# Optimization experiments

Hardware: AMD Instinct MI355X
Metric: run time of the kernel (lower is better)

The kernel has to match this reference:

```python
import jax, jax.numpy as jnp
import numpy as np
from jax import lax

T, IN, H, OUT = 8192, 1, 1024, 1


def setup_inputs() -> dict:
    key = jax.random.key(0)
    ks = jax.random.split(key, 7)
    s = 1.0 / np.sqrt(H)
    return {
        "x": jax.random.normal(ks[0], (T, IN), dtype=jnp.float32),
        "W_ih": jax.random.uniform(ks[1], (4 * H, IN), jnp.float32, -s, s),
        "W_hh": jax.random.uniform(ks[2], (4 * H, H), jnp.float32, -s, s),
        "b_ih": jax.random.uniform(ks[3], (4 * H,), jnp.float32, -s, s),
        "b_hh": jax.random.uniform(ks[4], (4 * H,), jnp.float32, -s, s),
        "W_fc": jax.random.uniform(ks[5], (OUT, H), jnp.float32, -s, s),
        "b_fc": jax.random.uniform(ks[6], (OUT,), jnp.float32, -s, s),
    }


def reference(x, W_ih, W_hh, b_ih, b_hh, W_fc, b_fc):
    # x: (T, input_size); batch dim of 1 is squeezed out.
    H_ = W_hh.shape[1]
    # Precompute input contribution to all gates for every timestep: (T, 4H)
    xg = x @ W_ih.T + (b_ih + b_hh)

    def step(carry, gx):
        h, c = carry
        g = gx + h @ W_hh.T  # (4H,) -- PyTorch gate order i, f, g, o
        i, f, gg, o = jnp.split(g, 4)
        c = jax.nn.sigmoid(f) * c + jax.nn.sigmoid(i) * jnp.tanh(gg)
        h = jax.nn.sigmoid(o) * jnp.tanh(c)
        return (h, c), h

    h0 = jnp.zeros((H_,), dtype=x.dtype)
    c0 = jnp.zeros((H_,), dtype=x.dtype)
    _, hs = lax.scan(step, (h0, c0), xg)  # hs: (T, H)
    return hs @ W_fc.T + b_fc  # (T, output_size)
```

## Files before the change

kernel.cpp:

```cpp
#include <hip/hip_runtime.h>

#define TT    8192
#define HD    1024
#define NBLK  256
#define NTHR  256
#define NBUF  4
#define NREP  8

typedef int i32x4 __attribute__((ext_vector_type(4)));
typedef int i32x2 __attribute__((ext_vector_type(2)));

__device__ __forceinline__ void llc_load_pair(const unsigned* p, i32x4& a, i32x4& b) {
  asm volatile("global_load_dwordx4 %0, %2, off sc0 sc1\n\t"
               "global_load_dwordx4 %1, %3, off sc0 sc1\n\t"
               "s_waitcnt vmcnt(0)"
               : "=&v"(a), "=&v"(b)
               : "v"(p), "v"(p + 4)
               : "memory");
}
__device__ __forceinline__ unsigned llc_load1(const unsigned* p) {
  unsigned r;
  asm volatile("global_load_dword %0, %1, off sc0 sc1\n\ts_waitcnt vmcnt(0)"
               : "=v"(r) : "v"(p) : "memory");
  return r;
}
__device__ __forceinline__ void llc_store2(unsigned* p, unsigned lo, unsigned hi) {
  i32x2 v; v.x = (int)lo; v.y = (int)hi;
  asm volatile("global_store_dwordx2 %0, %1, off sc0 sc1"
               :: "v"(p), "v"(v) : "memory");
}
__device__ __forceinline__ void llc_store1(unsigned* p, unsigned v) {
  asm volatile("global_store_dword %0, %1, off sc0 sc1"
               :: "v"(p), "v"(v) : "memory");
}

__device__ __forceinline__ float sigf(float z) {
  return 1.0f / (1.0f + __expf(-z));
}
__device__ __forceinline__ float tanh_fast(float z) {
  float az = fabsf(z);
  float e  = __expf(2.0f * az);
  float t  = 1.0f - 2.0f / (e + 1.0f);
  return z < 0.0f ? -t : t;
}

#define FMA4(acc, hvv, wvv)                                      \
  acc = fmaf((hvv).x, (wvv).x, acc);                             \
  acc = fmaf((hvv).y, (wvv).y, acc);                             \
  acc = fmaf((hvv).z, (wvv).z, acc);                             \
  acc = fmaf((hvv).w, (wvv).w, acc);

extern "C" __global__ __launch_bounds__(NTHR, 1)
void lstm_persistent(const float* __restrict__ x,
                     const float* __restrict__ W_ih,
                     const float* __restrict__ W_hh,
                     const float* __restrict__ b_ih,
                     const float* __restrict__ b_hh,
                     const float* __restrict__ W_fc,
                     const float* __restrict__ b_fc,
                     float* __restrict__ out,
                     unsigned* __restrict__ flag,
                     unsigned* __restrict__ hbuf)
{
  const int tid = threadIdx.x;
  const int blk = blockIdx.x;

  if (blk == NBLK) {
    for (int t = 0; t < TT; ++t) {
      const unsigned* src = hbuf + (((t & (NBUF - 1)) * HD + tid * 4) * 2);
      i32x4 A, B;
      const int want = t + 1;
      do {
        llc_load_pair(src, A, B);
      } while (!(A.y == want && A.w == want && B.y == want && B.w == want));
      __syncthreads();
      if (tid < NREP)
        llc_store1(flag + (tid << 4), (unsigned)want);
    }
    return;
  }

  __shared__ float x_lds[TT];
  __shared__ float h_lds[HD];

  const int wave = tid >> 6;
  const int lane = tid & 63;
  const int g    = lane >> 4;
  const int kc   = lane & 15;
  const int unit = blk * 4 + wave;

  for (int i = tid; i < TT / 4; i += NTHR)
    ((float4*)x_lds)[i] = ((const float4*)x)[i];

  float4 w4[16];
  {
    const float* wr = W_hh + (size_t)(g * HD + unit) * HD + kc * 4;
#pragma unroll
    for (int m = 0; m < 16; ++m)
      w4[m] = *((const float4*)(wr + m * 64));
  }
  float4 wfc4[4];
#pragma unroll
  for (int m = 0; m < 4; ++m)
    wfc4[m] = *((const float4*)(W_fc + m * 256 + lane * 4));
  const float bfc_val = b_fc[0];

  float wih_g[4], bs_g[4];
#pragma unroll
  for (int q = 0; q < 4; ++q) {
    int r = q * HD + unit;
    wih_g[q] = W_ih[r];
    bs_g[q]  = b_ih[r] + b_hh[r];
  }
  float c_state = 0.0f;
  __syncthreads();

  const unsigned* flag_mine = flag + ((blk & (NREP - 1)) << 4);

  for (int t = 0; t < TT; ++t) {
    const bool doproj = (t > 0) && (wave == 1) && (blk == (t & 255));
    float accs = 0.0f;
    float4 hp4[4];

    if (t > 0) {
      while (llc_load1(flag_mine) < (unsigned)t) { }
      const unsigned* src = hbuf + (((t - 1) & (NBUF - 1)) * HD + tid * 4) * 2;
      i32x4 A, B;
      llc_load_pair(src, A, B);
      float4 hv;
      hv.x = __int_as_float(A.x); hv.y = __int_as_float(A.z);
      hv.z = __int_as_float(B.x); hv.w = __int_as_float(B.z);
      ((float4*)h_lds)[tid] = hv;
      __syncthreads();

      const float* hp = h_lds + kc * 4;
      float s0 = 0.f, s1 = 0.f, s2 = 0.f, s3 = 0.f;
#pragma unroll
      for (int mb = 0; mb < 4; ++mb) {
        float4 ha = *((const float4*)(hp + (mb * 4 + 0) * 64));
        float4 hb = *((const float4*)(hp + (mb * 4 + 1) * 64));
        float4 hc = *((const float4*)(hp + (mb * 4 + 2) * 64));
        float4 hd = *((const float4*)(hp + (mb * 4 + 3) * 64));
        FMA4(s0, ha, w4[mb * 4 + 0]);
        FMA4(s1, hb, w4[mb * 4 + 1]);
        FMA4(s2, hc, w4[mb * 4 + 2]);
        FMA4(s3, hd, w4[mb * 4 + 3]);
      }
      accs = (s0 + s1) + (s2 + s3);

      if (doproj) {
#pragma unroll
        for (int m = 0; m < 4; ++m)
          hp4[m] = *((const float4*)(h_lds + m * 256 + lane * 4));
      }
    }

#pragma unroll
    for (int s = 1; s < 16; s <<= 1)
      accs += __shfl_xor(accs, s);

    float xt = x_lds[t];
    float a  = accs + fmaf(xt, wih_g[g], bs_g[g]);
    float act = (g == 2) ? tanh_fast(a) : sigf(a);

    float si = __shfl(act, 0);
    float sf = __shfl(act, 16);
    float sg = __shfl(act, 32);
    float so = __shfl(act, 48);

    if (lane == 0) {
      c_state  = sf * c_state + si * sg;
      float hn = so * tanh_fast(c_state);
      llc_store2(hbuf + (((t & (NBUF - 1)) * HD + unit) * 2),
                 __float_as_uint(hn), (unsigned)(t + 1));
    }

    if (doproj) {
      float p = 0.f;
#pragma unroll
      for (int m = 0; m < 4; ++m) { FMA4(p, hp4[m], wfc4[m]); }
#pragma unroll
      for (int s = 1; s < 64; s <<= 1) p += __shfl_xor(p, s);
      if (lane == 0) out[t - 1] = p + bfc_val;
    }
  }

  if (blk == 0) {
    const unsigned* src = hbuf + (((TT - 1) & (NBUF - 1)) * HD + tid * 4) * 2;
    i32x4 A, B;
    do {
      llc_load_pair(src, A, B);
    } while (!(A.y == TT && A.w == TT && B.y == TT && B.w == TT));
    float4 hv;
    hv.x = __int_as_float(A.x); hv.y = __int_as_float(A.z);
    hv.z = __int_as_float(B.x); hv.w = __int_as_float(B.z);
    ((float4*)h_lds)[tid] = hv;
    __syncthreads();
    if (wave == 1) {
      float p = 0.f;
#pragma unroll
      for (int m = 0; m < 4; ++m) {
        float4 hm = *((const float4*)(h_lds + m * 256 + lane * 4));
        FMA4(p, hm, wfc4[m]);
      }
#pragma unroll
      for (int s = 1; s < 64; s <<= 1) p += __shfl_xor(p, s);
      if (lane == 0) out[TT - 1] = p + bfc_val;
    }
  }
}

extern "C" void kernel_launch(void* const* d_in, const int* in_sizes, int n_in,
                              void* d_out, int out_size, void* d_ws, size_t ws_size,
                              hipStream_t stream) {
  const float* x   = (const float*)d_in[0];
  const float* Wih = (const float*)d_in[1];
  const float* Whh = (const float*)d_in[2];
  const float* bih = (const float*)d_in[3];
  const float* bhh = (const float*)d_in[4];
  const float* Wfc = (const float*)d_in[5];
  const float* bfc = (const float*)d_in[6];
  float* out = (float*)d_out;

  unsigned* flag = (unsigned*)d_ws;
  unsigned* hbuf = flag + NREP * 16;
  size_t init_bytes = (NREP * 16 + NBUF * HD * 2) * sizeof(unsigned);

  hipMemsetAsync(d_ws, 0, init_bytes, stream);
  hipLaunchKernelGGL(lstm_persistent, dim3(NBLK + 1), dim3(NTHR), 0, stream,
                     x, Wih, Whh, bih, bhh, Wfc, bfc, out, flag, hbuf);
}
```

Before: 23.23 ms.

## Speculatively poll tagged h buffer and distribute output projection via atomics

Each block first polls the tagged hidden-state entries directly, up to KSPEC attempts, and falls back to the aggregator flag only if that fails. This aims to remove the extra hop through the aggregator block from the per-step critical path. Each block's own h values are taken from LDS instead of global memory. The serial output projection, previously done by one rotating block, becomes per-block partial dot products accumulated with atomicAdd into a zeroed output. The cost is an extra __syncthreads per step, 256 atomics per timestep on the same address, and heavier polling traffic on the LLC.

```diff
diff --git a/kernel.cpp b/kernel.cpp
--- a/kernel.cpp
+++ b/kernel.cpp
@@ -6,6 +6,7 @@
 #define NTHR  256
 #define NBUF  4
 #define NREP  8
+#define KSPEC 4
 
 typedef int i32x4 __attribute__((ext_vector_type(4)));
 typedef int i32x2 __attribute__((ext_vector_type(2)));
@@ -69,19 +70,21 @@
     for (int t = 0; t < TT; ++t) {
       const unsigned* src = hbuf + (((t & (NBUF - 1)) * HD + tid * 4) * 2);
       i32x4 A, B;
-      const int want = t + 1;
+      const unsigned want = (unsigned)(t + 1);
       do {
         llc_load_pair(src, A, B);
-      } while (!(A.y == want && A.w == want && B.y == want && B.w == want));
+      } while (!((unsigned)A.y >= want && (unsigned)A.w >= want &&
+                 (unsigned)B.y >= want && (unsigned)B.w >= want));
       __syncthreads();
       if (tid < NREP)
-        llc_store1(flag + (tid << 4), (unsigned)want);
+        llc_store1(flag + (tid << 4), want);
     }
     return;
   }
 
   __shared__ float x_lds[TT];
   __shared__ float h_lds[HD];
+  __shared__ float own_h[4];
 
   const int wave = tid >> 6;
   const int lane = tid & 63;
@@ -99,12 +102,6 @@
     for (int m = 0; m < 16; ++m)
       w4[m] = *((const float4*)(wr + m * 64));
   }
-  float4 wfc4[4];
-#pragma unroll
-  for (int m = 0; m < 4; ++m)
-    wfc4[m] = *((const float4*)(W_fc + m * 256 + lane * 4));
-  const float bfc_val = b_fc[0];
-
   float wih_g[4], bs_g[4];
 #pragma unroll
   for (int q = 0; q < 4; ++q) {
@@ -112,24 +109,42 @@
     wih_g[q] = W_ih[r];
     bs_g[q]  = b_ih[r] + b_hh[r];
   }
+  float wfco[4];
+#pragma unroll
+  for (int q = 0; q < 4; ++q) wfco[q] = W_fc[blk * 4 + q];
+  const float bfc_add = (blk == 0) ? b_fc[0] : 0.0f;
+
   float c_state = 0.0f;
   __syncthreads();
 
   const unsigned* flag_mine = flag + ((blk & (NREP - 1)) << 4);
 
   for (int t = 0; t < TT; ++t) {
-    const bool doproj = (t > 0) && (wave == 1) && (blk == (t & 255));
     float accs = 0.0f;
-    float4 hp4[4];
 
     if (t > 0) {
-      while (llc_load1(flag_mine) < (unsigned)t) { }
-      const unsigned* src = hbuf + (((t - 1) & (NBUF - 1)) * HD + tid * 4) * 2;
-      i32x4 A, B;
-      llc_load_pair(src, A, B);
+      const unsigned want = (unsigned)t;
       float4 hv;
-      hv.x = __int_as_float(A.x); hv.y = __int_as_float(A.z);
-      hv.z = __int_as_float(B.x); hv.w = __int_as_float(B.z);
+      if (tid == blk) {
+        hv.x = own_h[0]; hv.y = own_h[1]; hv.z = own_h[2]; hv.w = own_h[3];
+      } else {
+        const unsigned* src =
+            hbuf + (((t - 1) & (NBUF - 1)) * HD + tid * 4) * 2;
+        i32x4 A, B;
+        bool ok;
+        int att = 0;
+        do {
+          llc_load_pair(src, A, B);
+          ok = ((unsigned)A.y == want && (unsigned)A.w == want &&
+                (unsigned)B.y == want && (unsigned)B.w == want);
+        } while (!ok && ++att < KSPEC);
+        if (!ok) {
+          while (llc_load1(flag_mine) < want) { }
+          llc_load_pair(src, A, B);
+        }
+        hv.x = __int_as_float(A.x); hv.y = __int_as_float(A.z);
+        hv.z = __int_as_float(B.x); hv.w = __int_as_float(B.z);
+      }
       ((float4*)h_lds)[tid] = hv;
       __syncthreads();
 
@@ -147,12 +162,6 @@
         FMA4(s3, hd, w4[mb * 4 + 3]);
       }
       accs = (s0 + s1) + (s2 + s3);
-
-      if (doproj) {
-#pragma unroll
-        for (int m = 0; m < 4; ++m)
-          hp4[m] = *((const float4*)(h_lds + m * 256 + lane * 4));
-      }
     }
 
 #pragma unroll
@@ -173,39 +182,15 @@
       float hn = so * tanh_fast(c_state);
       llc_store2(hbuf + (((t & (NBUF - 1)) * HD + unit) * 2),
                  __float_as_uint(hn), (unsigned)(t + 1));
-    }
-
-    if (doproj) {
-      float p = 0.f;
-#pragma unroll
-      for (int m = 0; m < 4; ++m) { FMA4(p, hp4[m], wfc4[m]); }
-#pragma unroll
-      for (int s = 1; s < 64; s <<= 1) p += __shfl_xor(p, s);
-      if (lane == 0) out[t - 1] = p + bfc_val;
-    }
-  }
-
-  if (blk == 0) {
-    const unsigned* src = hbuf + (((TT - 1) & (NBUF - 1)) * HD + tid * 4) * 2;
-    i32x4 A, B;
-    do {
-      llc_load_pair(src, A, B);
-    } while (!(A.y == TT && A.w == TT && B.y == TT && B.w == TT));
-    float4 hv;
-    hv.x = __int_as_float(A.x); hv.y = __int_as_float(A.z);
-    hv.z = __int_as_float(B.x); hv.w = __int_as_float(B.z);
-    ((float4*)h_lds)[tid] = hv;
+      own_h[wave] = hn;
+    }
+
     __syncthreads();
-    if (wave == 1) {
-      float p = 0.f;
-#pragma unroll
-      for (int m = 0; m < 4; ++m) {
-        float4 hm = *((const float4*)(h_lds + m * 256 + lane * 4));
-        FMA4(p, hm, wfc4[m]);
-      }
-#pragma unroll
-      for (int s = 1; s < 64; s <<= 1) p += __shfl_xor(p, s);
-      if (lane == 0) out[TT - 1] = p + bfc_val;
+
+    if (tid == 0) {
+      float part = own_h[0] * wfco[0] + own_h[1] * wfco[1] +
+                   own_h[2] * wfco[2] + own_h[3] * wfco[3] + bfc_add;
+      atomicAdd(out + t, part);
     }
   }
 }
@@ -227,6 +212,7 @@
   size_t init_bytes = (NREP * 16 + NBUF * HD * 2) * sizeof(unsigned);
 
   hipMemsetAsync(d_ws, 0, init_bytes, stream);
+  hipMemsetAsync(d_out, 0, (size_t)TT * sizeof(float), stream);
   hipLaunchKernelGGL(lstm_persistent, dim3(NBLK + 1), dim3(NTHR), 0, stream,
                      x, Wih, Whh, bih, bhh, Wfc, bfc, out, flag, hbuf);
 }
```

Result: slower. 32.74 ms (+41.0%).
